# Performance work log

Measured on AMD Instinct MI355X. Metric: run time of the kernel, lower is better.

## Reference

```python
import jax, jax.numpy as jnp
import numpy as np
import math

B, S, D, H = 2, 2048, 1024, 16
HD = D // H  # head dim = 64


def setup_inputs() -> dict:
    key = jax.random.key(0)
    k1, k2, k3, k4, k5 = jax.random.split(key, 5)
    query = jax.random.normal(k1, (B, S, D), dtype=jnp.float32)
    # tail padding: sequence lengths 1536 and 1792 -> positions >= length are padded (True)
    lengths = jnp.array([1536, 1792], dtype=jnp.int32)
    padding_mask = jnp.arange(S, dtype=jnp.int32)[None, :] >= lengths[:, None]  # [B,S] bool
    qkv_w = jax.random.normal(k2, (3 * D, D), dtype=jnp.float32) * 0.02
    qkv_b = jax.random.uniform(k3, (3 * D,), dtype=jnp.float32, minval=-0.03, maxval=0.03)
    out_w = jax.random.normal(k4, (D, D), dtype=jnp.float32) * 0.02
    out_b = jax.random.uniform(k5, (D,), dtype=jnp.float32, minval=-0.03, maxval=0.03)
    return {"query": query, "padding_mask": padding_mask,
            "qkv_w": qkv_w, "qkv_b": qkv_b, "out_w": out_w, "out_b": out_b}


def reference(query, padding_mask, qkv_w, qkv_b, out_w, out_b):
    # self-attention path (qkv_same=True): fused qkv projection then split
    qkv = query @ qkv_w.T + qkv_b                      # [B,S,3D]
    q, k, v = jnp.split(qkv, 3, axis=-1)               # each [B,S,D]

    def split_heads(x):
        return x.reshape(B, S, H, HD).transpose(0, 2, 1, 3)  # [B,H,S,HD]

    q, k, v = split_heads(q), split_heads(k), split_heads(v)

    # scores scaled by sqrt(head_dim)
    w = jnp.einsum('bhqd,bhkd->bhqk', q, k) / math.sqrt(HD)  # [B,H,S,S]

    # causal (future) mask: strict upper triangle masked
    future = jnp.triu(jnp.ones((S, S), dtype=bool), 1)
    w = jnp.where(future[None, None, :, :], -jnp.inf, w)
    # key padding mask
    w = jnp.where(padding_mask[:, None, None, :], -jnp.inf, w)

    a = jax.nn.softmax(w, axis=-1)
    # rows of fully-padded sequences are zeroed (dropout is identity in eval)
    all_masked = jnp.all(padding_mask, axis=-1)        # [B]
    a = jnp.where(all_masked[:, None, None, None], 0.0, a)

    x = jnp.einsum('bhqk,bhkd->bhqd', a, v)            # [B,H,S,HD]
    x = x.transpose(0, 2, 1, 3).reshape(B, S, D)       # merge heads
    return x @ out_w.T + out_b
```

## Files before the change

kernel.cpp:

```cpp
#include <hip/hip_runtime.h>
#include <hip/hip_bf16.h>
#include <stdint.h>

#define S_  2048
#define B_  2
#define H_  16
#define D_  1024
#define HD_ 64

typedef short short8 __attribute__((ext_vector_type(8)));
typedef float f32x4  __attribute__((ext_vector_type(4)));

__device__ __forceinline__ unsigned short bf16_rne(float f) {
  unsigned int u = __float_as_uint(f);
  u += 0x7fffu + ((u >> 16) & 1u);
  return (unsigned short)(u >> 16);
}

__device__ __forceinline__ f32x4 mfma_bf16(short8 a, short8 b, f32x4 c) {
  return __builtin_amdgcn_mfma_f32_16x16x32_bf16(a, b, c, 0, 0, 0);
}

__global__ void cvt3_kernel(const float* __restrict__ a, unsigned short* __restrict__ oa, int na8,
                            const float* __restrict__ b, unsigned short* __restrict__ ob, int nb8,
                            const float* __restrict__ c, unsigned short* __restrict__ oc, int nc8) {
  int i = blockIdx.x * blockDim.x + threadIdx.x;
  const float* in; unsigned short* out; int idx;
  if (i < na8) { in = a; out = oa; idx = i; }
  else if (i < na8 + nb8) { in = b; out = ob; idx = i - na8; }
  else if (i < na8 + nb8 + nc8) { in = c; out = oc; idx = i - na8 - nb8; }
  else return;
  const float4* p = (const float4*)in + (size_t)idx * 2;
  float4 x = p[0], y = p[1];
  union { unsigned short u[8]; short8 v; } r;
  r.u[0] = bf16_rne(x.x); r.u[1] = bf16_rne(x.y);
  r.u[2] = bf16_rne(x.z); r.u[3] = bf16_rne(x.w);
  r.u[4] = bf16_rne(y.x); r.u[5] = bf16_rne(y.y);
  r.u[6] = bf16_rne(y.z); r.u[7] = bf16_rne(y.w);
  *((short8*)out + idx) = r.v;
}

__global__ void lengths_kernel(const void* __restrict__ mask, int* __restrict__ lens) {
  __shared__ int mn[B_];
  __shared__ int anyb;
  int t = threadIdx.x;
  if (t < B_) mn[t] = S_;
  if (t == 0) anyb = 0;
  __syncthreads();
  const unsigned char* mb = (const unsigned char*)mask;
  for (int i = t; i < B_ * S_; i += 256) {
    if (mb[i]) { anyb = 1; atomicMin(&mn[i >> 11], i & (S_ - 1)); }
  }
  __syncthreads();
  if (!anyb) {
    const int* mi = (const int*)mask;
    for (int i = t; i < B_ * S_; i += 256) {
      if (mi[i]) atomicMin(&mn[i >> 11], i & (S_ - 1));
    }
    __syncthreads();
  }
  if (t < B_) lens[t] = mn[t];
}

__global__ __launch_bounds__(512, 2) void gemm8p_kernel(
    const unsigned short* __restrict__ A,
    const unsigned short* __restrict__ W,
    int K, int NBX,
    const float* __restrict__ bias,
    unsigned short* __restrict__ qb,
    unsigned short* __restrict__ kb,
    unsigned short* __restrict__ vb) {
  __shared__ __align__(16) unsigned short lds[65536];

  const int nwg = gridDim.x;
  const int cpx = nwg >> 3;
  const int bid = blockIdx.x;
  const int virt = (bid & 7) * cpx + (bid >> 3);
  const int bx = virt % NBX, by = virt / NBX;
  const int tile_m = by * 256, tile_n = bx * 256;
  const int t = threadIdx.x;
  const int lane = t & 63, w = t >> 6;
  const int wm = w >> 2, wn = w & 3;
  const int l15 = lane & 15, lk = lane >> 4;
  const int NT = K >> 6;

  f32x4 acc[8][4];
#pragma unroll
  for (int i = 0; i < 8; i++)
#pragma unroll
    for (int j = 0; j < 4; j++) { f32x4 z = {0.f, 0.f, 0.f, 0.f}; acc[i][j] = z; }

  const int L0 = t, L1 = 512 + t;
  const int r0 = L0 >> 3, c0 = (L0 & 7) ^ (r0 & 7);
  const int r1 = L1 >> 3, c1 = (L1 & 7) ^ (r1 & 7);

#define STAGE_HALF(SRC, GROW0, DSTE, KC)                                      \
  {                                                                           \
    __builtin_amdgcn_global_load_lds(                                         \
        (const __attribute__((address_space(1))) void*)(                      \
            (SRC) + (size_t)((GROW0) + r0) * K + (KC) + c0 * 8),              \
        (__attribute__((address_space(3))) void*)(&lds[(DSTE) + L0 * 8]),     \
        16, 0, 0);                                                            \
    __builtin_amdgcn_global_load_lds(                                         \
        (const __attribute__((address_space(1))) void*)(                      \
            (SRC) + (size_t)((GROW0) + r1) * K + (KC) + c1 * 8),              \
        (__attribute__((address_space(3))) void*)(&lds[(DSTE) + L1 * 8]),     \
        16, 0, 0);                                                            \
  }

  STAGE_HALF(A, tile_m,        0,    0);
  STAGE_HALF(W, tile_n,        32768, 0);
  STAGE_HALF(A, tile_m + 128,  8192, 0);
  STAGE_HALF(W, tile_n + 128,  32768 + 8192, 0);
  asm volatile("s_waitcnt vmcnt(4)" ::: "memory");
  __builtin_amdgcn_s_barrier();

  for (int tc = 0; tc < NT; ++tc) {
    const int cb = (tc & 1) * 16384;
    const int ob = ((tc & 1) ^ 1) * 16384;
    int tn = tc + 1; if (tn >= NT) tn = NT - 1;
    const int k0n = tn << 6;

#pragma unroll
    for (int p = 0; p < 4; ++p) {
      const int mh = (p & 1);
      const int nh = (p >> 1);
      short8 af[4][2], bfr[2][2];
#pragma unroll
      for (int fi = 0; fi < 4; ++fi) {
        const int rl = fi * 32 + wm * 16 + l15;
#pragma unroll
        for (int ks = 0; ks < 2; ++ks) {
          const int sw = (ks * 4 + lk) ^ (rl & 7);
          af[fi][ks] = *(const short8*)&lds[cb + mh * 8192 + rl * 64 + sw * 8];
        }
      }
#pragma unroll
      for (int fj = 0; fj < 2; ++fj) {
        const int cl = wn * 32 + fj * 16 + l15;
#pragma unroll
        for (int ks = 0; ks < 2; ++ks) {
          const int sw = (ks * 4 + lk) ^ (cl & 7);
          bfr[fj][ks] =
              *(const short8*)&lds[32768 + cb + nh * 8192 + cl * 64 + sw * 8];
        }
      }
      if (p == 0)      STAGE_HALF(A, tile_m,       ob,                k0n)
      else if (p == 1) STAGE_HALF(W, tile_n,       32768 + ob,        k0n)
      else if (p == 2) STAGE_HALF(A, tile_m + 128, ob + 8192,         k0n)
      else             STAGE_HALF(W, tile_n + 128, 32768 + ob + 8192, k0n);
      if (p != 2) asm volatile("s_waitcnt vmcnt(4)" ::: "memory");
      else        asm volatile("" ::: "memory");
      __builtin_amdgcn_s_barrier();
      asm volatile("s_waitcnt lgkmcnt(0)" ::: "memory");
      __builtin_amdgcn_s_setprio(1);
#pragma unroll
      for (int fi = 0; fi < 4; ++fi)
#pragma unroll
        for (int fj = 0; fj < 2; ++fj)
#pragma unroll
          for (int ks = 0; ks < 2; ++ks)
            acc[mh * 4 + fi][nh * 2 + fj] =
                mfma_bf16(af[fi][ks], bfr[fj][ks], acc[mh * 4 + fi][nh * 2 + fj]);
      __builtin_amdgcn_s_setprio(0);
      __builtin_amdgcn_s_barrier();
    }
  }
  asm volatile("s_waitcnt vmcnt(0)" ::: "memory");
#undef STAGE_HALF

#pragma unroll
  for (int j = 0; j < 4; ++j) {
    const int gn = tile_n + (j >> 1) * 128 + wn * 32 + (j & 1) * 16 + l15;
    const float bv = bias[gn];
    const int which = gn >> 10, dd = gn & (D_ - 1);
    const int h = dd >> 6, d = dd & 63;
    unsigned short* dstp = (which == 0) ? qb : (which == 1) ? kb : vb;
    const float mul = (which == 0) ? 0.125f : 1.0f;
#pragma unroll
    for (int i = 0; i < 8; ++i) {
      const int gmb = tile_m + (i >> 2) * 128 + (i & 3) * 32 + wm * 16 + lk * 4;
#pragma unroll
      for (int r = 0; r < 4; ++r) {
        const int gm = gmb + r;
        const int bb = gm >> 11, s = gm & (S_ - 1);
        dstp[((size_t)((bb * H_ + h) * S_ + s)) * HD_ + d] =
            bf16_rne((acc[i][j][r] + bv) * mul);
      }
    }
  }
}

__global__ __launch_bounds__(256) void gemm_bt_kernel(
    const unsigned short* __restrict__ A,
    const unsigned short* __restrict__ W,
    int K, int N,
    const float* __restrict__ bias,
    float* __restrict__ outf) {
  __shared__ unsigned short As[128 * 32];
  __shared__ unsigned short Bs[128 * 32];
  const int tile_m = blockIdx.y * 128;
  const int tile_n = blockIdx.x * 128;
  const int t = threadIdx.x;
  const int lane = t & 63;
  const int w = t >> 6;
  const int wr = w >> 1, wc = w & 1;
  const int l15 = lane & 15, lk = lane >> 4;

  f32x4 acc[4][4];
#pragma unroll
  for (int i = 0; i < 4; i++)
#pragma unroll
    for (int j = 0; j < 4; j++) { f32x4 z = {0.f, 0.f, 0.f, 0.f}; acc[i][j] = z; }

  for (int k0 = 0; k0 < K; k0 += 32) {
#pragma unroll
    for (int c = 0; c < 2; ++c) {
      int e = (c * 256 + t) * 8;
      int row = e >> 5, col = e & 31;
      __builtin_amdgcn_global_load_lds(
          (__attribute__((address_space(1))) void*)(A + (size_t)(tile_m + row) * K + k0 + col),
          (__attribute__((address_space(3))) void*)(&As[e]), 16, 0, 0);
      __builtin_amdgcn_global_load_lds(
          (__attribute__((address_space(1))) void*)(W + (size_t)(tile_n + row) * K + k0 + col),
          (__attribute__((address_space(3))) void*)(&Bs[e]), 16, 0, 0);
    }
    asm volatile("s_waitcnt vmcnt(0)" ::: "memory");
    __syncthreads();

    short8 af[4], bfr[4];
#pragma unroll
    for (int i = 0; i < 4; i++)
      af[i] = *(const short8*)&As[(wr * 64 + i * 16 + l15) * 32 + lk * 8];
#pragma unroll
    for (int j = 0; j < 4; j++)
      bfr[j] = *(const short8*)&Bs[(wc * 64 + j * 16 + l15) * 32 + lk * 8];
#pragma unroll
    for (int i = 0; i < 4; i++)
#pragma unroll
      for (int j = 0; j < 4; j++)
        acc[i][j] = mfma_bf16(af[i], bfr[j], acc[i][j]);
    __syncthreads();
  }

#pragma unroll
  for (int i = 0; i < 4; i++) {
#pragma unroll
    for (int j = 0; j < 4; j++) {
      int gn = tile_n + wc * 64 + j * 16 + l15;
      float bv = bias[gn];
#pragma unroll
      for (int r = 0; r < 4; r++) {
        int gm = tile_m + wr * 64 + i * 16 + lk * 4 + r;
        outf[(size_t)gm * N + gn] = acc[i][j][r] + bv;
      }
    }
  }
}

__global__ __launch_bounds__(512) void attn_kernel(
    const unsigned short* __restrict__ qbuf,
    const unsigned short* __restrict__ kbuf,
    const unsigned short* __restrict__ vbuf,
    const int* __restrict__ lens,
    unsigned short* __restrict__ attn_out) {
  __shared__ __align__(16) char smem[51200];

  const int bid = blockIdx.x;
  const int virt = ((bid & 7) << 7) | (bid >> 3);
  const int bh = virt >> 5;
  const int qt = virt & 31;
  const int b = bh >> 4;
  const int len = lens[b];
  const int t = threadIdx.x;
  const int lane = t & 63, w = t >> 6;
  const int g = w >> 2, wg = w & 3;
  const int l15 = lane & 15, lk = lane >> 4;
  const int qbase = qt * 64 + wg * 16;

  unsigned short* Ks = (unsigned short*)(smem + g * 8192);
  unsigned int*   Vt = (unsigned int*)(smem + 16384 + g * 9216);
  unsigned short* Ps = (unsigned short*)(smem + 34816 + (w << 11));

  const unsigned short* qbh = qbuf + (size_t)bh * S_ * HD_;
  const unsigned short* kbh = kbuf + (size_t)bh * S_ * HD_;
  const unsigned short* vbh = vbuf + (size_t)bh * S_ * HD_;

  const int qrow = qbase + l15;
  const short8 qf0 = *(const short8*)&qbh[(size_t)qrow * HD_ + lk * 8];
  const short8 qf1 = *(const short8*)&qbh[(size_t)qrow * HD_ + 32 + lk * 8];

  f32x4 o[4];
#pragma unroll
  for (int n = 0; n < 4; n++) { f32x4 z = {0.f, 0.f, 0.f, 0.f}; o[n] = z; }
  float rsum[4] = {0.f, 0.f, 0.f, 0.f};

  const int ke = (len - 1) >> 6;
  const int kt_end = qt < ke ? qt : ke;
  const int NI = (kt_end >> 1) + 1;

  const int tg = t & 255;
  const int vr2 = tg & 31, vcg = tg >> 5;
  const int kr0 = tg >> 3, kc0 = tg & 7;

  short8 pk0 = {}, pk1 = {}, pv0 = {}, pv1 = {};

#define LDG(KT)                                                               \
  {                                                                           \
    int ks0_ = (KT) * 64;                                                     \
    pk0 = *(const short8*)&kbh[(size_t)(ks0_ + kr0) * HD_ + kc0 * 8];         \
    pk1 = *(const short8*)&kbh[(size_t)(ks0_ + kr0 + 32) * HD_ + kc0 * 8];    \
    const unsigned short* vp = vbh + (size_t)(ks0_ + 2 * vr2) * HD_ + vcg * 8;\
    pv0 = *(const short8*)vp;                                                 \
    pv1 = *(const short8*)(vp + HD_);                                         \
  }

  int my_kt = g;
  bool act = (my_kt <= kt_end);
  if (act) LDG(my_kt);

  for (int i = 0; i < NI; ++i) {
    __syncthreads();
    if (act) {
      *(short8*)&Ks[kr0 * 64 + ((kc0 ^ (kr0 & 7)) << 3)] = pk0;
      int r1 = kr0 + 32;
      *(short8*)&Ks[r1 * 64 + ((kc0 ^ (r1 & 7)) << 3)] = pk1;
#pragma unroll
      for (int j = 0; j < 8; j++) {
        int d = vcg * 8 + j;
        unsigned int pk = (unsigned int)(unsigned short)pv0[j] |
                          ((unsigned int)(unsigned short)pv1[j] << 16);
        Vt[d * 36 + ((((vr2 >> 1) ^ (d & 15)) << 1) | (vr2 & 1))] = pk;
      }
    }
    __syncthreads();
    const int nxt = my_kt + 2;
    const bool nact = (nxt <= kt_end);
    if (nact) LDG(nxt);

    if (act) {
      const int ks0 = my_kt * 64;
      f32x4 sc[4];
#pragma unroll
      for (int j = 0; j < 4; j++) {
        int krow = j * 16 + l15;
        const short8 kf0 =
            *(const short8*)&Ks[krow * 64 + ((lk ^ (krow & 7)) << 3)];
        const short8 kf1 =
            *(const short8*)&Ks[krow * 64 + (((4 | lk) ^ (krow & 7)) << 3)];
        f32x4 a = {0.f, 0.f, 0.f, 0.f};
        a = mfma_bf16(qf0, kf0, a);
        a = mfma_bf16(qf1, kf1, a);
        sc[j] = a;
      }
      if ((my_kt == qt) || (ks0 + 63 >= len)) {
#pragma unroll
        for (int j = 0; j < 4; j++)
#pragma unroll
          for (int r = 0; r < 4; r++) {
            int q = qbase + lk * 4 + r;
            int kk = ks0 + j * 16 + l15;
            if (kk > q || kk >= len) sc[j][r] = -1e30f;
          }
      }
#pragma unroll
      for (int j = 0; j < 4; j++)
#pragma unroll
        for (int r = 0; r < 4; r++) {
          float p = __expf(sc[j][r]);
          rsum[r] += p;
          int qr = lk * 4 + r;
          Ps[qr * 64 + ((j * 16 + l15) ^ ((qr & 7) << 3))] = bf16_rne(p);
        }
#pragma unroll
      for (int ks2 = 0; ks2 < 2; ++ks2) {
        const short8 pf = *(const short8*)
            &Ps[l15 * 64 + ((ks2 * 32 + lk * 8) ^ ((l15 & 7) << 3))];
        const int g0 = ks2 * 8 + lk * 2;
#pragma unroll
        for (int n = 0; n < 4; n++) {
          int d = n * 16 + l15;
          uint2 w0 = *(const uint2*)&Vt[d * 36 + ((g0 ^ l15) << 1)];
          uint2 w1 = *(const uint2*)&Vt[d * 36 + (((g0 + 1) ^ l15) << 1)];
          union { unsigned int u[4]; short8 s; } vv;
          vv.u[0] = w0.x; vv.u[1] = w0.y; vv.u[2] = w1.x; vv.u[3] = w1.y;
          o[n] = mfma_bf16(pf, vv.s, o[n]);
        }
      }
    }
    my_kt = nxt; act = nact;
  }
#undef LDG

#pragma unroll
  for (int r = 0; r < 4; r++) {
#pragma unroll
    for (int d = 1; d < 16; d <<= 1) rsum[r] += __shfl_xor(rsum[r], d, 64);
  }

  float* mo = (float*)smem;
  float* ml = (float*)(smem + 16896);
  __syncthreads();
  if (g == 1) {
#pragma unroll
    for (int r = 0; r < 4; r++) {
      int row = wg * 16 + lk * 4 + r;
#pragma unroll
      for (int n = 0; n < 4; n++) mo[row * 66 + n * 16 + l15] = o[n][r];
      if (l15 == 0) ml[row] = rsum[r];
    }
  }
  __syncthreads();
  if (g == 0) {
#pragma unroll
    for (int r = 0; r < 4; r++) {
      int row = wg * 16 + lk * 4 + r;
      float lt = rsum[r] + ml[row];
      float inv = (lt > 0.f) ? (1.0f / lt) : 0.f;
      int s = qt * 64 + row;
#pragma unroll
      for (int n = 0; n < 4; n++) {
        float ot = o[n][r] + mo[row * 66 + n * 16 + l15];
        attn_out[((size_t)(b * S_ + s)) * D_ + (bh & 15) * HD_ + n * 16 + l15] =
            bf16_rne(ot * inv);
      }
    }
  }
}

extern "C" void kernel_launch(void* const* d_in, const int* in_sizes, int n_in,
                              void* d_out, int out_size, void* d_ws, size_t ws_size,
                              hipStream_t stream) {
  const float* query = (const float*)d_in[0];
  const void*  mask  = d_in[1];
  const float* qkv_w = (const float*)d_in[2];
  const float* qkv_b = (const float*)d_in[3];
  const float* out_w = (const float*)d_in[4];
  const float* out_b = (const float*)d_in[5];
  float* out = (float*)d_out;

  char* ws = (char*)d_ws;
  unsigned short* qx     = (unsigned short*)(ws);
  unsigned short* wqkv   = (unsigned short*)(ws + (8u  << 20));
  unsigned short* wout   = (unsigned short*)(ws + (14u << 20));
  unsigned short* qbuf   = (unsigned short*)(ws + (16u << 20));
  unsigned short* kbuf   = (unsigned short*)(ws + (24u << 20));
  unsigned short* vbuf   = (unsigned short*)(ws + (32u << 20));
  unsigned short* attn_o = qx;
  int* lens              = (int*)(ws + (40u << 20));

  lengths_kernel<<<1, 256, 0, stream>>>(mask, lens);
  const int na8 = B_ * S_ * D_ / 8, nb8 = 3 * D_ * D_ / 8, nc8 = D_ * D_ / 8;
  cvt3_kernel<<<(na8 + nb8 + nc8) / 256, 256, 0, stream>>>(
      query, qx, na8, qkv_w, wqkv, nb8, out_w, wout, nc8);

  gemm8p_kernel<<<192, 512, 0, stream>>>(qx, wqkv, D_, 3 * D_ / 256, qkv_b,
                                         qbuf, kbuf, vbuf);

  attn_kernel<<<1024, 512, 0, stream>>>(qbuf, kbuf, vbuf, lens, attn_o);

  dim3 g2(D_ / 128, B_ * S_ / 128);
  gemm_bt_kernel<<<g2, 256, 0, stream>>>(attn_o, wout, D_, D_, out_b, out);
}
```

Measured before the change: 147.0 us.

## Rework attention kernel to 32x32 MFMA with register-resident P via permlane swaps

The attention kernel moves from 16x16x32 MFMA tiles to 32x32x16 MFMA tiles, computing S transposed so each lane holds one query's scores. The probability tile is packed with v_cvt_pk_bf16 and rearranged with v_permlane32_swap instead of going through a shared-memory P buffer. Blocks shrink to 256 threads with launch bounds for three blocks per CU, and fully masked 32-key halves above the causal diagonal are skipped. This cuts LDS traffic and the row-sum shuffles, but relies on gfx950-specific instructions and increases register pressure per thread.

```diff
diff --git a/kernel.cpp b/kernel.cpp
--- a/kernel.cpp
+++ b/kernel.cpp
@@ -10,6 +10,7 @@
 
 typedef short short8 __attribute__((ext_vector_type(8)));
 typedef float f32x4  __attribute__((ext_vector_type(4)));
+typedef float f32x16 __attribute__((ext_vector_type(16)));
 
 __device__ __forceinline__ unsigned short bf16_rne(float f) {
   unsigned int u = __float_as_uint(f);
@@ -19,6 +20,16 @@
 
 __device__ __forceinline__ f32x4 mfma_bf16(short8 a, short8 b, f32x4 c) {
   return __builtin_amdgcn_mfma_f32_16x16x32_bf16(a, b, c, 0, 0, 0);
+}
+
+__device__ __forceinline__ f32x16 mfma32(short8 a, short8 b, f32x16 c) {
+  return __builtin_amdgcn_mfma_f32_32x32x16_bf16(a, b, c, 0, 0, 0);
+}
+
+__device__ __forceinline__ unsigned int cvtpk_bf16(float lo, float hi) {
+  unsigned int r;
+  asm("v_cvt_pk_bf16_f32 %0, %1, %2" : "=v"(r) : "v"(lo), "v"(hi));
+  return r;
 }
 
 __global__ void cvt3_kernel(const float* __restrict__ a, unsigned short* __restrict__ oa, int na8,
@@ -258,13 +269,14 @@
   }
 }
 
-__global__ __launch_bounds__(512) void attn_kernel(
+__global__ __launch_bounds__(256, 3) void attn_kernel(
     const unsigned short* __restrict__ qbuf,
     const unsigned short* __restrict__ kbuf,
     const unsigned short* __restrict__ vbuf,
     const int* __restrict__ lens,
     unsigned short* __restrict__ attn_out) {
-  __shared__ __align__(16) char smem[51200];
+  __shared__ __align__(16) char smem[33792];
+  __shared__ float lsh[2][64];
 
   const int bid = blockIdx.x;
   const int virt = ((bid & 7) << 7) | (bid >> 3);
@@ -274,63 +286,73 @@
   const int len = lens[b];
   const int t = threadIdx.x;
   const int lane = t & 63, w = t >> 6;
-  const int g = w >> 2, wg = w & 3;
-  const int l15 = lane & 15, lk = lane >> 4;
-  const int qbase = qt * 64 + wg * 16;
+  const int g = w >> 1, wq = w & 1;
+  const int l31 = lane & 31, hi = lane >> 5;
+  const int hi8 = hi * 8, hi4 = hi * 4;
+  const int q0 = qt * 64 + wq * 32;
+  const int qme = q0 + l31;
 
   unsigned short* Ks = (unsigned short*)(smem + g * 8192);
-  unsigned int*   Vt = (unsigned int*)(smem + 16384 + g * 9216);
-  unsigned short* Ps = (unsigned short*)(smem + 34816 + (w << 11));
+  unsigned int*   Vt = (unsigned int*)(smem + 16384 + g * 8704);
 
   const unsigned short* qbh = qbuf + (size_t)bh * S_ * HD_;
   const unsigned short* kbh = kbuf + (size_t)bh * S_ * HD_;
   const unsigned short* vbh = vbuf + (size_t)bh * S_ * HD_;
 
-  const int qrow = qbase + l15;
-  const short8 qf0 = *(const short8*)&qbh[(size_t)qrow * HD_ + lk * 8];
-  const short8 qf1 = *(const short8*)&qbh[(size_t)qrow * HD_ + 32 + lk * 8];
-
-  f32x4 o[4];
-#pragma unroll
-  for (int n = 0; n < 4; n++) { f32x4 z = {0.f, 0.f, 0.f, 0.f}; o[n] = z; }
-  float rsum[4] = {0.f, 0.f, 0.f, 0.f};
+  short8 qf[4];
+#pragma unroll
+  for (int ds = 0; ds < 4; ++ds)
+    qf[ds] = *(const short8*)&qbh[(size_t)(q0 + l31) * HD_ + ds * 16 + hi8];
+
+  f32x16 o[2] = {{}, {}};
+  float rsum = 0.f;
 
   const int ke = (len - 1) >> 6;
   const int kt_end = qt < ke ? qt : ke;
   const int NI = (kt_end >> 1) + 1;
 
-  const int tg = t & 255;
-  const int vr2 = tg & 31, vcg = tg >> 5;
+  const int tg = t & 127;
   const int kr0 = tg >> 3, kc0 = tg & 7;
-
-  short8 pk0 = {}, pk1 = {}, pv0 = {}, pv1 = {};
+  const int vr2 = tg & 31, vcb = (tg >> 5) << 1;
+
+  short8 pk[4], pva0 = {}, pva1 = {}, pvb0 = {}, pvb1 = {};
+#pragma unroll
+  for (int m = 0; m < 4; ++m) pk[m] = pva0;
 
 #define LDG(KT)                                                               \
   {                                                                           \
-    int ks0_ = (KT) * 64;                                                     \
-    pk0 = *(const short8*)&kbh[(size_t)(ks0_ + kr0) * HD_ + kc0 * 8];         \
-    pk1 = *(const short8*)&kbh[(size_t)(ks0_ + kr0 + 32) * HD_ + kc0 * 8];    \
-    const unsigned short* vp = vbh + (size_t)(ks0_ + 2 * vr2) * HD_ + vcg * 8;\
-    pv0 = *(const short8*)vp;                                                 \
-    pv1 = *(const short8*)(vp + HD_);                                         \
+    int ks_ = (KT) * 64;                                                      \
+    pk[0] = *(const short8*)&kbh[(size_t)(ks_ + kr0     ) * HD_ + kc0 * 8];   \
+    pk[1] = *(const short8*)&kbh[(size_t)(ks_ + kr0 + 16) * HD_ + kc0 * 8];   \
+    pk[2] = *(const short8*)&kbh[(size_t)(ks_ + kr0 + 32) * HD_ + kc0 * 8];   \
+    pk[3] = *(const short8*)&kbh[(size_t)(ks_ + kr0 + 48) * HD_ + kc0 * 8];   \
+    const unsigned short* vp = vbh + (size_t)(ks_ + 2 * vr2) * HD_ + vcb * 8; \
+    pva0 = *(const short8*)vp;       pva1 = *(const short8*)(vp + HD_);       \
+    pvb0 = *(const short8*)(vp + 8); pvb1 = *(const short8*)(vp + HD_ + 8);   \
   }
 
   int my_kt = g;
   bool act = (my_kt <= kt_end);
   if (act) LDG(my_kt);
 
+  typedef union { unsigned int u[4]; short8 s; } pa_t;
+
   for (int i = 0; i < NI; ++i) {
     __syncthreads();
     if (act) {
-      *(short8*)&Ks[kr0 * 64 + ((kc0 ^ (kr0 & 7)) << 3)] = pk0;
-      int r1 = kr0 + 32;
-      *(short8*)&Ks[r1 * 64 + ((kc0 ^ (r1 & 7)) << 3)] = pk1;
-#pragma unroll
-      for (int j = 0; j < 8; j++) {
-        int d = vcg * 8 + j;
-        unsigned int pk = (unsigned int)(unsigned short)pv0[j] |
-                          ((unsigned int)(unsigned short)pv1[j] << 16);
-        Vt[d * 36 + ((((vr2 >> 1) ^ (d & 15)) << 1) | (vr2 & 1))] = pk;
+#pragma unroll
+      for (int m = 0; m < 4; ++m) {
+        const int r = kr0 + 16 * m;
+        *(short8*)&Ks[r * 64 + ((kc0 ^ (r & 7)) << 3)] = pk[m];
+      }
+#pragma unroll
+      for (int j = 0; j < 8; ++j) {
+        unsigned int w0 = (unsigned int)(unsigned short)pva0[j] |
+                          ((unsigned int)(unsigned short)pva1[j] << 16);
+        unsigned int w1 = (unsigned int)(unsigned short)pvb0[j] |
+                          ((unsigned int)(unsigned short)pvb1[j] << 16);
+        Vt[(vcb * 8 + j) * 34 + vr2] = w0;
+        Vt[((vcb + 1) * 8 + j) * 34 + vr2] = w1;
       }
     }
     __syncthreads();
@@ -338,53 +360,91 @@
     const bool nact = (nxt <= kt_end);
     if (nact) LDG(nxt);
 
-    if (act) {
-      const int ks0 = my_kt * 64;
-      f32x4 sc[4];
-#pragma unroll
-      for (int j = 0; j < 4; j++) {
-        int krow = j * 16 + l15;
-        const short8 kf0 =
-            *(const short8*)&Ks[krow * 64 + ((lk ^ (krow & 7)) << 3)];
-        const short8 kf1 =
-            *(const short8*)&Ks[krow * 64 + (((4 | lk) ^ (krow & 7)) << 3)];
-        f32x4 a = {0.f, 0.f, 0.f, 0.f};
-        a = mfma_bf16(qf0, kf0, a);
-        a = mfma_bf16(qf1, kf1, a);
-        sc[j] = a;
-      }
-      if ((my_kt == qt) || (ks0 + 63 >= len)) {
-#pragma unroll
-        for (int j = 0; j < 4; j++)
-#pragma unroll
-          for (int r = 0; r < 4; r++) {
-            int q = qbase + lk * 4 + r;
-            int kk = ks0 + j * 16 + l15;
-            if (kk > q || kk >= len) sc[j][r] = -1e30f;
+    const int ks0 = my_kt * 64;
+    if (act && ks0 <= q0 + 31) {
+      const bool needM = (ks0 + 63 >= q0) || (ks0 + 63 >= len);
+      const bool dokb1 = (ks0 + 32 <= q0 + 31) && (ks0 + 32 < len);
+
+      pa_t pa[4];
+      {
+        f32x16 s0 = {};
+#pragma unroll
+        for (int ds = 0; ds < 4; ++ds) {
+          const int cg = ((ds << 1) | hi) ^ (l31 & 7);
+          const short8 kf = *(const short8*)&Ks[l31 * 64 + (cg << 3)];
+          s0 = mfma32(kf, qf[ds], s0);
+        }
+        float pr[16];
+#pragma unroll
+        for (int r = 0; r < 16; ++r) {
+          const int crow = (r & 3) + 8 * (r >> 2) + hi4;
+          float p = __expf(s0[r]);
+          if (needM) {
+            const int key = ks0 + crow;
+            if (key > qme || key >= len) p = 0.f;
           }
-      }
-#pragma unroll
-      for (int j = 0; j < 4; j++)
-#pragma unroll
-        for (int r = 0; r < 4; r++) {
-          float p = __expf(sc[j][r]);
-          rsum[r] += p;
-          int qr = lk * 4 + r;
-          Ps[qr * 64 + ((j * 16 + l15) ^ ((qr & 7) << 3))] = bf16_rne(p);
-        }
-#pragma unroll
-      for (int ks2 = 0; ks2 < 2; ++ks2) {
-        const short8 pf = *(const short8*)
-            &Ps[l15 * 64 + ((ks2 * 32 + lk * 8) ^ ((l15 & 7) << 3))];
-        const int g0 = ks2 * 8 + lk * 2;
-#pragma unroll
-        for (int n = 0; n < 4; n++) {
-          int d = n * 16 + l15;
-          uint2 w0 = *(const uint2*)&Vt[d * 36 + ((g0 ^ l15) << 1)];
-          uint2 w1 = *(const uint2*)&Vt[d * 36 + (((g0 + 1) ^ l15) << 1)];
-          union { unsigned int u[4]; short8 s; } vv;
-          vv.u[0] = w0.x; vv.u[1] = w0.y; vv.u[2] = w1.x; vv.u[3] = w1.y;
-          o[n] = mfma_bf16(pf, vv.s, o[n]);
+          pr[r] = p; rsum += p;
+        }
+        unsigned int A0 = cvtpk_bf16(pr[0], pr[1]);
+        unsigned int A1 = cvtpk_bf16(pr[2], pr[3]);
+        unsigned int B0 = cvtpk_bf16(pr[4], pr[5]);
+        unsigned int B1 = cvtpk_bf16(pr[6], pr[7]);
+        asm volatile("v_permlane32_swap_b32 %0, %1" : "+v"(A0), "+v"(B0));
+        asm volatile("v_permlane32_swap_b32 %0, %1" : "+v"(A1), "+v"(B1));
+        pa[0].u[0] = A0; pa[0].u[1] = A1; pa[0].u[2] = B0; pa[0].u[3] = B1;
+        unsigned int C0 = cvtpk_bf16(pr[8], pr[9]);
+        unsigned int C1 = cvtpk_bf16(pr[10], pr[11]);
+        unsigned int D0 = cvtpk_bf16(pr[12], pr[13]);
+        unsigned int D1 = cvtpk_bf16(pr[14], pr[15]);
+        asm volatile("v_permlane32_swap_b32 %0, %1" : "+v"(C0), "+v"(D0));
+        asm volatile("v_permlane32_swap_b32 %0, %1" : "+v"(C1), "+v"(D1));
+        pa[1].u[0] = C0; pa[1].u[1] = C1; pa[1].u[2] = D0; pa[1].u[3] = D1;
+      }
+      if (dokb1) {
+        f32x16 s1 = {};
+#pragma unroll
+        for (int ds = 0; ds < 4; ++ds) {
+          const int cg = ((ds << 1) | hi) ^ (l31 & 7);
+          const short8 kf = *(const short8*)&Ks[(32 + l31) * 64 + (cg << 3)];
+          s1 = mfma32(kf, qf[ds], s1);
+        }
+        float pr[16];
+#pragma unroll
+        for (int r = 0; r < 16; ++r) {
+          const int crow = 32 + (r & 3) + 8 * (r >> 2) + hi4;
+          float p = __expf(s1[r]);
+          if (needM) {
+            const int key = ks0 + crow;
+            if (key > qme || key >= len) p = 0.f;
+          }
+          pr[r] = p; rsum += p;
+        }
+        unsigned int A0 = cvtpk_bf16(pr[0], pr[1]);
+        unsigned int A1 = cvtpk_bf16(pr[2], pr[3]);
+        unsigned int B0 = cvtpk_bf16(pr[4], pr[5]);
+        unsigned int B1 = cvtpk_bf16(pr[6], pr[7]);
+        asm volatile("v_permlane32_swap_b32 %0, %1" : "+v"(A0), "+v"(B0));
+        asm volatile("v_permlane32_swap_b32 %0, %1" : "+v"(A1), "+v"(B1));
+        pa[2].u[0] = A0; pa[2].u[1] = A1; pa[2].u[2] = B0; pa[2].u[3] = B1;
+        unsigned int C0 = cvtpk_bf16(pr[8], pr[9]);
+        unsigned int C1 = cvtpk_bf16(pr[10], pr[11]);
+        unsigned int D0 = cvtpk_bf16(pr[12], pr[13]);
+        unsigned int D1 = cvtpk_bf16(pr[14], pr[15]);
+        asm volatile("v_permlane32_swap_b32 %0, %1" : "+v"(C0), "+v"(D0));
+        asm volatile("v_permlane32_swap_b32 %0, %1" : "+v"(C1), "+v"(D1));
+        pa[3].u[0] = C0; pa[3].u[1] = C1; pa[3].u[2] = D0; pa[3].u[3] = D1;
+      }
+#pragma unroll
+      for (int dh = 0; dh < 2; ++dh) {
+        const int vbase = (dh * 32 + l31) * 34 + hi4;
+#pragma unroll
+        for (int ks = 0; ks < 4; ++ks) {
+          if (ks >= 2 && !dokb1) continue;
+          uint2 va = *(const uint2*)&Vt[vbase + 8 * ks];
+          uint2 vb2 = *(const uint2*)&Vt[vbase + 8 * ks + 2];
+          pa_t vv;
+          vv.u[0] = va.x; vv.u[1] = va.y; vv.u[2] = vb2.x; vv.u[3] = vb2.y;
+          o[dh] = mfma32(pa[ks].s, vv.s, o[dh]);
         }
       }
     }
@@ -392,38 +452,34 @@
   }
 #undef LDG
 
-#pragma unroll
-  for (int r = 0; r < 4; r++) {
-#pragma unroll
-    for (int d = 1; d < 16; d <<= 1) rsum[r] += __shfl_xor(rsum[r], d, 64);
-  }
+  rsum += __shfl_xor(rsum, 32, 64);
 
   float* mo = (float*)smem;
-  float* ml = (float*)(smem + 16896);
   __syncthreads();
   if (g == 1) {
 #pragma unroll
-    for (int r = 0; r < 4; r++) {
-      int row = wg * 16 + lk * 4 + r;
-#pragma unroll
-      for (int n = 0; n < 4; n++) mo[row * 66 + n * 16 + l15] = o[n][r];
-      if (l15 == 0) ml[row] = rsum[r];
-    }
+    for (int r = 0; r < 16; ++r) {
+      const int qb = wq * 32 + (r & 3) + 8 * (r >> 2) + hi4;
+      mo[qb * 66 + l31]      = o[0][r];
+      mo[qb * 66 + 32 + l31] = o[1][r];
+    }
+    if (hi == 0) lsh[1][wq * 32 + l31] = rsum;
   }
   __syncthreads();
   if (g == 0) {
-#pragma unroll
-    for (int r = 0; r < 4; r++) {
-      int row = wg * 16 + lk * 4 + r;
-      float lt = rsum[r] + ml[row];
-      float inv = (lt > 0.f) ? (1.0f / lt) : 0.f;
-      int s = qt * 64 + row;
-#pragma unroll
-      for (int n = 0; n < 4; n++) {
-        float ot = o[n][r] + mo[row * 66 + n * 16 + l15];
-        attn_out[((size_t)(b * S_ + s)) * D_ + (bh & 15) * HD_ + n * 16 + l15] =
-            bf16_rne(ot * inv);
-      }
+    const float lt = rsum + lsh[1][wq * 32 + l31];
+    const float inv = (lt > 0.f) ? (1.0f / lt) : 0.f;
+    if (hi == 0) lsh[0][wq * 32 + l31] = inv;
+#pragma unroll
+    for (int r = 0; r < 16; ++r) {
+      const int cr = (r & 3) + 8 * (r >> 2) + hi4;
+      const int qb = wq * 32 + cr;
+      const float iv = lsh[0][wq * 32 + cr];
+      const int s = qt * 64 + qb;
+      unsigned short* op =
+          &attn_out[((size_t)(b * S_ + s)) * D_ + (bh & 15) * HD_ + l31];
+      op[0]  = bf16_rne((o[0][r] + mo[qb * 66 + l31]) * iv);
+      op[32] = bf16_rne((o[1][r] + mo[qb * 66 + 32 + l31]) * iv);
     }
   }
 }
@@ -457,7 +513,7 @@
   gemm8p_kernel<<<192, 512, 0, stream>>>(qx, wqkv, D_, 3 * D_ / 256, qkv_b,
                                          qbuf, kbuf, vbuf);
 
-  attn_kernel<<<1024, 512, 0, stream>>>(qbuf, kbuf, vbuf, lens, attn_o);
+  attn_kernel<<<1024, 256, 0, stream>>>(qbuf, kbuf, vbuf, lens, attn_o);
 
   dim3 g2(D_ / 128, B_ * S_ / 128);
   gemm_bt_kernel<<<g2, 256, 0, stream>>>(attn_o, wout, D_, D_, out_b, out);
```

Measured after the change: 144.0 us. -2.1%, faster.
